# Optimization experiments

Measured on AMD Instinct MI355X. Metric: run time of the kernel, lower is better.

## Reference

```python
import jax, jax.numpy as jnp
import numpy as np

EMB_DIM = 512
R_DIM = 64
B, S = 8, 2048


def _lowrank_params(key):
    k1, k2, k3, k4 = jax.random.split(key, 4)
    s1 = 1.0 / np.sqrt(EMB_DIM)
    s2 = 1.0 / np.sqrt(R_DIM)
    w1 = jax.random.uniform(k1, (EMB_DIM, R_DIM), jnp.float32, -s1, s1)
    b1 = jax.random.uniform(k2, (R_DIM,), jnp.float32, -s1, s1)
    w2 = jax.random.uniform(k3, (R_DIM, EMB_DIM), jnp.float32, -s2, s2)
    b2 = jax.random.uniform(k4, (EMB_DIM,), jnp.float32, -s2, s2)
    return w1, b1, w2, b2


def setup_inputs() -> dict:
    key = jax.random.key(0)
    kx, km, kq, kk, kv = jax.random.split(key, 5)
    x = jax.random.normal(kx, (B, S, EMB_DIM), jnp.float32)
    attention_mask = jax.random.randint(km, (B, S), 0, 2, jnp.int32)
    q_w1, q_b1, q_w2, q_b2 = _lowrank_params(kq)
    k_w1, k_b1, k_w2, k_b2 = _lowrank_params(kk)
    v_w1, v_b1, v_w2, v_b2 = _lowrank_params(kv)
    return dict(x=x, attention_mask=attention_mask,
                q_w1=q_w1, q_b1=q_b1, q_w2=q_w2, q_b2=q_b2,
                k_w1=k_w1, k_b1=k_b1, k_w2=k_w2, k_b2=k_b2,
                v_w1=v_w1, v_b1=v_b1, v_w2=v_w2, v_b2=v_b2)


def _proj(x, w1, b1, w2, b2):
    # low-rank projection: emb -> r -> emb (two stacked Linears, no nonlinearity)
    return (x @ w1 + b1) @ w2 + b2


def reference(x, attention_mask,
              q_w1, q_b1, q_w2, q_b2,
              k_w1, k_b1, k_w2, k_b2,
              v_w1, v_b1, v_w2, v_b2):
    q = _proj(x, q_w1, q_b1, q_w2, q_b2)   # [B,S,E]
    k = _proj(x, k_w1, k_b1, k_w2, k_b2)   # [B,S,E]
    v = _proj(x, v_w1, v_b1, v_w2, v_b2)   # [B,S,E]
    scale = EMB_DIM ** (-0.5)
    scores = jnp.einsum('bse,bte->bst', q, k) * scale  # [B,S,S]
    m = attention_mask.astype(jnp.float32)
    scores = scores * m[:, :, None] * m[:, None, :]
    temp = jnp.einsum('bst,bte->bse', scores, v)       # [B,S,E]
    out = jax.nn.softmax(temp, axis=-1)                # softmax AFTER second bmm (non-standard)
    return out, q
```

## Files before the change

kernel.cpp:

```cpp
#include <hip/hip_runtime.h>
#include <hip/hip_bf16.h>

#define SCALE 0.044194173824159216f

typedef float f32x4 __attribute__((ext_vector_type(4)));
typedef __bf16 bf16x8 __attribute__((ext_vector_type(8)));

static __device__ __forceinline__ unsigned short f2bf(float f){
  unsigned u = __builtin_bit_cast(unsigned, f);
  u += 0x7fffu + ((u >> 16) & 1u);
  return (unsigned short)(u >> 16);
}

__global__ __launch_bounds__(256) void kA(const float* __restrict__ w1q, const float* __restrict__ w1k,
    const float* __restrict__ w1v, const float* __restrict__ w2q, const float* __restrict__ b2q,
    const float* __restrict__ w2k, const float* __restrict__ b2k,
    const float* __restrict__ w2v, const float* __restrict__ b2v,
    unsigned short* __restrict__ W1T, unsigned short* __restrict__ W2qT, float* __restrict__ Pm,
    unsigned short* __restrict__ Wvb){
  const int bid = blockIdx.x, t = threadIdx.x;
  if (bid < 64){
    #pragma unroll
    for (int s = 0; s < 8; s++){
      int id = s*16384 + bid*256 + t;
      if (id < 192*512){
        int n = id >> 9, k = id & 511;
        int p = n >> 6, c = n & 63;
        const float* w1 = (p==0)? w1q : ((p==1)? w1k : w1v);
        W1T[id] = f2bf(w1[k*64 + c]);
      } else {
        int j = id - 192*512;
        int e = j >> 6, r = j & 63;
        W2qT[j] = f2bf(w2q[r*512 + e]);
      }
    }
  } else if (bid < 81){
    int id = (bid - 64)*256 + t;
    if (id < 65*65){
      int i = id / 65, j = id - i*65;
      const float* qi = (i < 64)? (w2q + i*512) : b2q;
      const float* kj = (j < 64)? (w2k + j*512) : b2k;
      float s = 0.f;
      for (int e = 0; e < 512; e += 4){
        float4 a = *(const float4*)(qi + e);
        float4 b = *(const float4*)(kj + e);
        s += a.x*b.x + a.y*b.y + a.z*b.z + a.w*b.w;
      }
      Pm[id] = s * SCALE;
    }
  } else {
    int e = (bid - 81)*256 + t;
    unsigned short* wp = Wvb + e*96;
    for (int k = 0; k < 64; k++) wp[k] = f2bf(w2v[k*512 + e]);
    wp[64] = f2bf(b2v[e]);
    #pragma unroll
    for (int k = 65; k < 96; k++) wp[k] = 0;
  }
}

__global__ __launch_bounds__(256) void kB(const float* __restrict__ x, const unsigned short* __restrict__ W1T,
    const float* __restrict__ b1q, const float* __restrict__ b1k, const float* __restrict__ b1v,
    const int* __restrict__ mask,
    unsigned short* __restrict__ Hq, float* __restrict__ part){
  __shared__ __attribute__((aligned(16))) char smem[33792];
  unsigned short (*Ax)[40] = (unsigned short(*)[40])smem;
  unsigned short (*Bt)[40] = (unsigned short(*)[40])(smem + 5120);
  float (*ak)[66] = (float(*)[66])smem;
  float (*av)[66] = (float(*)[66])(smem + 16896);
  const int t = threadIdx.x;
  const int lane = t & 63, wave = t >> 6;
  const int l15 = lane & 15, lg = lane >> 4, ks = lg * 8;
  const int r0 = blockIdx.x * 64;
  f32x4 acc[12];
  #pragma unroll
  for (int j = 0; j < 12; j++) acc[j] = (f32x4){0.f,0.f,0.f,0.f};
  for (int k0 = 0; k0 < 512; k0 += 32){
    #pragma unroll
    for (int s = 0; s < 2; s++){
      int i = t + 256*s;
      int r = i >> 3, kq = (i & 7) * 4;
      float4 v = *(const float4*)(x + (size_t)(r0 + r)*512 + k0 + kq);
      ushort4 pk; pk.x = f2bf(v.x); pk.y = f2bf(v.y); pk.z = f2bf(v.z); pk.w = f2bf(v.w);
      *(ushort4*)&Ax[r][kq] = pk;
    }
    #pragma unroll
    for (int s = 0; s < 3; s++){
      int i = t + 256*s;
      int n = i >> 2, kq = (i & 3) * 8;
      *(uint4*)&Bt[n][kq] = *(const uint4*)(W1T + n*512 + k0 + kq);
    }
    __syncthreads();
    const int arow = (wave << 4) | l15;
    bf16x8 af = *(const bf16x8*)&Ax[arow][ks];
    #pragma unroll
    for (int j = 0; j < 12; j++){
      bf16x8 bf = *(const bf16x8*)&Bt[j*16 + l15][ks];
      acc[j] = __builtin_amdgcn_mfma_f32_16x16x32_bf16(af, bf, acc[j], 0, 0, 0);
    }
    __syncthreads();
  }
  int rowl[4]; float mrow[4];
  #pragma unroll
  for (int rg = 0; rg < 4; rg++){
    rowl[rg] = (wave << 4) + (lg << 2) + rg;
    mrow[rg] = (float)mask[r0 + rowl[rg]];
  }
  #pragma unroll
  for (int j = 0; j < 4; j++){
    int c = (j << 4) | l15;
    float bias = b1q[c];
    #pragma unroll
    for (int rg = 0; rg < 4; rg++)
      Hq[(size_t)(r0 + rowl[rg])*64 + c] = f2bf(acc[j][rg] + bias);
  }
  #pragma unroll
  for (int j = 0; j < 4; j++){
    int c = (j << 4) | l15;
    float bias = b1k[c];
    #pragma unroll
    for (int rg = 0; rg < 4; rg++)
      ak[rowl[rg]][c] = (acc[4 + j][rg] + bias) * mrow[rg];
  }
  #pragma unroll
  for (int j = 0; j < 4; j++){
    int c = (j << 4) | l15;
    float bias = b1v[c];
    #pragma unroll
    for (int rg = 0; rg < 4; rg++)
      av[rowl[rg]][c] = acc[8 + j][rg] + bias;
  }
  if (t < 64){ ak[t][64] = (float)mask[r0 + t]; av[t][64] = 1.f; }
  __syncthreads();
  if (t < 169){
    int tj = t / 13, ti = t - tj*13;
    int i0 = ti * 5, j0 = tj * 5;
    float pacc[5][5];
    #pragma unroll
    for (int a = 0; a < 5; a++)
      #pragma unroll
      for (int v = 0; v < 5; v++) pacc[a][v] = 0.f;
    for (int r = 0; r < 64; r++){
      float a[5], v[5];
      #pragma unroll
      for (int ii = 0; ii < 5; ii++) a[ii] = ak[r][i0 + ii];
      #pragma unroll
      for (int jj = 0; jj < 5; jj++) v[jj] = av[r][j0 + jj];
      #pragma unroll
      for (int ii = 0; ii < 5; ii++)
        #pragma unroll
        for (int jj = 0; jj < 5; jj++) pacc[ii][jj] += a[ii] * v[jj];
    }
    float* pout = part + (size_t)blockIdx.x * 4228;
    #pragma unroll
    for (int ii = 0; ii < 5; ii++)
      #pragma unroll
      for (int jj = 0; jj < 5; jj++)
        pout[(i0 + ii)*65 + (j0 + jj)] = pacc[ii][jj];
  }
}

__global__ __launch_bounds__(256) void kR2(const float* __restrict__ part, const float* __restrict__ Pm,
    unsigned short* __restrict__ T1bt, float* __restrict__ T1r64){
  __shared__ float Pl[65*66];
  __shared__ float Atl[4228];
  const int t = threadIdx.x, b = blockIdx.x;
  for (int id = t; id < 4225; id += 256){
    int i = id / 65, j = id - i*65;
    Pl[i*66 + j] = Pm[id];
  }
  const float* pb = part + (size_t)b*32*4228;
  for (int q = t; q < 1056; q += 256){
    f32x4 s0 = (f32x4){0.f,0.f,0.f,0.f}, s1 = s0, s2 = s0, s3 = s0;
    #pragma unroll
    for (int ch = 0; ch < 32; ch += 4){
      s0 += *(const f32x4*)(pb + (size_t)ch*4228     + q*4);
      s1 += *(const f32x4*)(pb + (size_t)(ch+1)*4228 + q*4);
      s2 += *(const f32x4*)(pb + (size_t)(ch+2)*4228 + q*4);
      s3 += *(const f32x4*)(pb + (size_t)(ch+3)*4228 + q*4);
    }
    *(f32x4*)&Atl[q*4] = (s0 + s1) + (s2 + s3);
  }
  if (t == 0){
    float s = 0.f;
    #pragma unroll
    for (int ch = 0; ch < 32; ch++) s += pb[(size_t)ch*4228 + 4224];
    Atl[4224] = s;
  }
  __syncthreads();
  unsigned short* Tb = T1bt + b*5120;
  float* Tr = T1r64 + b*80;
  if (t < 169){
    int tj = t / 13, ti = t - tj*13;
    int i0 = ti * 5, j0 = tj * 5;
    float acc[5][5];
    #pragma unroll
    for (int a = 0; a < 5; a++)
      #pragma unroll
      for (int v = 0; v < 5; v++) acc[a][v] = 0.f;
    for (int k = 0; k < 65; k++){
      float a[5], vv[5];
      #pragma unroll
      for (int ii = 0; ii < 5; ii++) a[ii] = Pl[(i0 + ii)*66 + k];
      #pragma unroll
      for (int jj = 0; jj < 5; jj++) vv[jj] = Atl[k*65 + j0 + jj];
      #pragma unroll
      for (int ii = 0; ii < 5; ii++)
        #pragma unroll
        for (int jj = 0; jj < 5; jj++) acc[ii][jj] += a[ii] * vv[jj];
    }
    #pragma unroll
    for (int ii = 0; ii < 5; ii++){
      int i = i0 + ii;
      #pragma unroll
      for (int jj = 0; jj < 5; jj++){
        int j = j0 + jj;
        if (i < 64) Tb[j*64 + i] = f2bf(acc[ii][jj]);
        else        Tr[j] = acc[ii][jj];
      }
    }
  }
  if (t < 240){
    int j = 65 + t/16, i4 = (t & 15) << 2;
    *(ushort4*)&Tb[j*64 + i4] = (ushort4){0,0,0,0};
  } else if (t < 255){
    Tr[65 + (t - 240)] = 0.f;
  }
}

__global__ __launch_bounds__(256) void kD2(const unsigned short* __restrict__ Hq,
    const unsigned short* __restrict__ W2qT, const unsigned short* __restrict__ T1bt,
    const float* __restrict__ T1r64, const unsigned short* __restrict__ Wvb,
    const float* __restrict__ b2q, const int* __restrict__ mask,
    float* __restrict__ out, float* __restrict__ qout){
  __shared__ __attribute__((aligned(16))) unsigned short t1l[64][104];
  const int t = threadIdx.x, lane = t & 63, wave = t >> 6;
  const int b = blockIdx.x >> 5, rc = (blockIdx.x & 31) << 6;
  const int l15 = lane & 15, lg = lane >> 4, ks = lg * 8;
  const size_t gr0 = (size_t)b*2048 + rc;
  const int arow = (wave << 4) | l15;
  const unsigned short* arp = Hq + (gr0 + arow)*64 + ks;
  bf16x8 a0 = *(const bf16x8*)arp;
  bf16x8 a1 = *(const bf16x8*)(arp + 32);
  const unsigned short* Tb = T1bt + b*5120;
  const float* Tr = T1r64 + b*80;
  f32x4 acc1[5];
  #pragma unroll
  for (int jf = 0; jf < 5; jf++) acc1[jf] = (f32x4){0.f,0.f,0.f,0.f};
  #pragma unroll
  for (int jf = 0; jf < 5; jf++){
    int col = (jf << 4) | l15;
    bf16x8 b0 = *(const bf16x8*)(Tb + col*64 + ks);
    bf16x8 b1 = *(const bf16x8*)(Tb + col*64 + 32 + ks);
    acc1[jf] = __builtin_amdgcn_mfma_f32_16x16x32_bf16(a0, b0, acc1[jf], 0, 0, 0);
    acc1[jf] = __builtin_amdgcn_mfma_f32_16x16x32_bf16(a1, b1, acc1[jf], 0, 0, 0);
  }
  *(ushort4*)&t1l[t >> 2][80 + ((t & 3) << 2)] = (ushort4){0,0,0,0};
  #pragma unroll
  for (int jf = 0; jf < 5; jf++){
    int col = (jf << 4) | l15;
    float tr = Tr[col];
    #pragma unroll
    for (int rg = 0; rg < 4; rg++)
      t1l[(wave << 4) + (lg << 2) + rg][col] = f2bf(acc1[jf][rg] + tr);
  }
  __syncthreads();
  bf16x8 c0 = *(const bf16x8*)&t1l[arow][ks];
  bf16x8 c1 = *(const bf16x8*)&t1l[arow][32 + ks];
  bf16x8 c2 = *(const bf16x8*)&t1l[arow][64 + ks];
  f32x4 acc[32];
  #pragma unroll
  for (int f = 0; f < 32; f++) acc[f] = (f32x4){0.f,0.f,0.f,0.f};
  #pragma unroll
  for (int f = 0; f < 32; f++){
    int col = (f << 4) | l15;
    const unsigned short* wp = Wvb + col*96;
    bf16x8 b0 = *(const bf16x8*)(wp + ks);
    bf16x8 b1 = *(const bf16x8*)(wp + 32 + ks);
    bf16x8 b2 = *(const bf16x8*)(wp + 64 + ks);
    acc[f] = __builtin_amdgcn_mfma_f32_16x16x32_bf16(c0, b0, acc[f], 0, 0, 0);
    acc[f] = __builtin_amdgcn_mfma_f32_16x16x32_bf16(c1, b1, acc[f], 0, 0, 0);
    acc[f] = __builtin_amdgcn_mfma_f32_16x16x32_bf16(c2, b2, acc[f], 0, 0, 0);
  }
  #pragma unroll
  for (int rg = 0; rg < 4; rg++){
    int row = rc + (wave << 4) + (lg << 2) + rg;
    float m = (float)mask[b*2048 + row];
    float mx = -3.4e38f;
    #pragma unroll
    for (int f = 0; f < 32; f++){
      float v = acc[f][rg] * m;
      acc[f][rg] = v;
      mx = fmaxf(mx, v);
    }
    #pragma unroll
    for (int d = 1; d < 16; d <<= 1) mx = fmaxf(mx, __shfl_xor(mx, d, 64));
    float sum = 0.f;
    #pragma unroll
    for (int f = 0; f < 32; f++){
      float ev = __expf(acc[f][rg] - mx);
      acc[f][rg] = ev;
      sum += ev;
    }
    #pragma unroll
    for (int d = 1; d < 16; d <<= 1) sum += __shfl_xor(sum, d, 64);
    float inv = 1.f / sum;
    float* orow = out + ((size_t)b*2048 + row) * 512;
    #pragma unroll
    for (int f = 0; f < 32; f++) orow[(f << 4) | l15] = acc[f][rg] * inv;
  }
  #pragma unroll
  for (int f = 0; f < 32; f++) acc[f] = (f32x4){0.f,0.f,0.f,0.f};
  #pragma unroll
  for (int f = 0; f < 32; f++){
    int col = (f << 4) | l15;
    bf16x8 b0 = *(const bf16x8*)(W2qT + col*64 + ks);
    bf16x8 b1 = *(const bf16x8*)(W2qT + col*64 + 32 + ks);
    acc[f] = __builtin_amdgcn_mfma_f32_16x16x32_bf16(a0, b0, acc[f], 0, 0, 0);
    acc[f] = __builtin_amdgcn_mfma_f32_16x16x32_bf16(a1, b1, acc[f], 0, 0, 0);
  }
  #pragma unroll
  for (int f = 0; f < 32; f++){
    int col = (f << 4) | l15;
    float bias = b2q[col];
    #pragma unroll
    for (int rg = 0; rg < 4; rg++){
      int row = rc + (wave << 4) + (lg << 2) + rg;
      qout[((size_t)b*2048 + row) * 512 + col] = acc[f][rg] + bias;
    }
  }
}

extern "C" void kernel_launch(void* const* d_in, const int* in_sizes, int n_in,
                              void* d_out, int out_size, void* d_ws, size_t ws_size,
                              hipStream_t stream){
  const float* x    = (const float*)d_in[0];
  const int*   mask = (const int*)d_in[1];
  const float* q_w1 = (const float*)d_in[2];
  const float* q_b1 = (const float*)d_in[3];
  const float* q_w2 = (const float*)d_in[4];
  const float* q_b2 = (const float*)d_in[5];
  const float* k_w1 = (const float*)d_in[6];
  const float* k_b1 = (const float*)d_in[7];
  const float* k_w2 = (const float*)d_in[8];
  const float* k_b2 = (const float*)d_in[9];
  const float* v_w1 = (const float*)d_in[10];
  const float* v_b1 = (const float*)d_in[11];
  const float* v_w2 = (const float*)d_in[12];
  const float* v_b2 = (const float*)d_in[13];

  char* ws = (char*)d_ws;
  unsigned short* W1T  = (unsigned short*)(ws + 0);
  unsigned short* W2qT = (unsigned short*)(ws + 196608);
  float*          Pm   = (float*)(ws + 262144);
  unsigned short* Hq   = (unsigned short*)(ws + 279296);
  float*          part = (float*)(ws + 2376448);
  unsigned short* Wvb  = (unsigned short*)(ws + 6705920);
  unsigned short* T1bt = (unsigned short*)(ws + 6804224);
  float*          T1r64= (float*)(ws + 6886144);

  float* out  = (float*)d_out;
  float* qout = out + (size_t)8*2048*512;

  kA <<<83,  256, 0, stream>>>(q_w1, k_w1, v_w1, q_w2, q_b2, k_w2, k_b2, v_w2, v_b2,
                               W1T, W2qT, Pm, Wvb);
  kB <<<256, 256, 0, stream>>>(x, W1T, q_b1, k_b1, v_b1, mask, Hq, part);
  kR2<<<8,   256, 0, stream>>>(part, Pm, T1bt, T1r64);
  kD2<<<256, 256, 0, stream>>>(Hq, W2qT, T1bt, T1r64, Wvb, q_b2, mask, out, qout);
}
```

Before: 93.65 us.

## Split reduction across many blocks and recompute small 65x65 product per block

```diff
diff --git a/kernel.cpp b/kernel.cpp
--- a/kernel.cpp
+++ b/kernel.cpp
@@ -10,6 +10,10 @@
   unsigned u = __builtin_bit_cast(unsigned, f);
   u += 0x7fffu + ((u >> 16) & 1u);
   return (unsigned short)(u >> 16);
+}
+static __device__ __forceinline__ __bf16 f2bfv(float f){
+  unsigned short s = f2bf(f);
+  return __builtin_bit_cast(__bf16, s);
 }
 
 __global__ __launch_bounds__(256) void kA(const float* __restrict__ w1q, const float* __restrict__ w1k,
@@ -159,80 +163,28 @@
   }
 }
 
-__global__ __launch_bounds__(256) void kR2(const float* __restrict__ part, const float* __restrict__ Pm,
-    unsigned short* __restrict__ T1bt, float* __restrict__ T1r64){
-  __shared__ float Pl[65*66];
-  __shared__ float Atl[4228];
-  const int t = threadIdx.x, b = blockIdx.x;
-  for (int id = t; id < 4225; id += 256){
-    int i = id / 65, j = id - i*65;
-    Pl[i*66 + j] = Pm[id];
-  }
-  const float* pb = part + (size_t)b*32*4228;
-  for (int q = t; q < 1056; q += 256){
-    f32x4 s0 = (f32x4){0.f,0.f,0.f,0.f}, s1 = s0, s2 = s0, s3 = s0;
-    #pragma unroll
-    for (int ch = 0; ch < 32; ch += 4){
-      s0 += *(const f32x4*)(pb + (size_t)ch*4228     + q*4);
-      s1 += *(const f32x4*)(pb + (size_t)(ch+1)*4228 + q*4);
-      s2 += *(const f32x4*)(pb + (size_t)(ch+2)*4228 + q*4);
-      s3 += *(const f32x4*)(pb + (size_t)(ch+3)*4228 + q*4);
-    }
-    *(f32x4*)&Atl[q*4] = (s0 + s1) + (s2 + s3);
-  }
-  if (t == 0){
+__global__ __launch_bounds__(256) void kR(const float* __restrict__ part, float* __restrict__ At){
+  int g = blockIdx.x*256 + threadIdx.x;
+  if (g < 33800){
+    int b = g / 4225, e = g - b*4225;
+    const float* p = part + (size_t)b*32*4228 + e;
     float s = 0.f;
     #pragma unroll
-    for (int ch = 0; ch < 32; ch++) s += pb[(size_t)ch*4228 + 4224];
-    Atl[4224] = s;
-  }
-  __syncthreads();
-  unsigned short* Tb = T1bt + b*5120;
-  float* Tr = T1r64 + b*80;
-  if (t < 169){
-    int tj = t / 13, ti = t - tj*13;
-    int i0 = ti * 5, j0 = tj * 5;
-    float acc[5][5];
-    #pragma unroll
-    for (int a = 0; a < 5; a++)
-      #pragma unroll
-      for (int v = 0; v < 5; v++) acc[a][v] = 0.f;
-    for (int k = 0; k < 65; k++){
-      float a[5], vv[5];
-      #pragma unroll
-      for (int ii = 0; ii < 5; ii++) a[ii] = Pl[(i0 + ii)*66 + k];
-      #pragma unroll
-      for (int jj = 0; jj < 5; jj++) vv[jj] = Atl[k*65 + j0 + jj];
-      #pragma unroll
-      for (int ii = 0; ii < 5; ii++)
-        #pragma unroll
-        for (int jj = 0; jj < 5; jj++) acc[ii][jj] += a[ii] * vv[jj];
-    }
-    #pragma unroll
-    for (int ii = 0; ii < 5; ii++){
-      int i = i0 + ii;
-      #pragma unroll
-      for (int jj = 0; jj < 5; jj++){
-        int j = j0 + jj;
-        if (i < 64) Tb[j*64 + i] = f2bf(acc[ii][jj]);
-        else        Tr[j] = acc[ii][jj];
-      }
-    }
-  }
-  if (t < 240){
-    int j = 65 + t/16, i4 = (t & 15) << 2;
-    *(ushort4*)&Tb[j*64 + i4] = (ushort4){0,0,0,0};
-  } else if (t < 255){
-    Tr[65 + (t - 240)] = 0.f;
-  }
-}
-
-__global__ __launch_bounds__(256) void kD2(const unsigned short* __restrict__ Hq,
-    const unsigned short* __restrict__ W2qT, const unsigned short* __restrict__ T1bt,
-    const float* __restrict__ T1r64, const unsigned short* __restrict__ Wvb,
+    for (int ch = 0; ch < 32; ch++) s += p[(size_t)ch*4228];
+    At[g] = s;
+  }
+}
+
+__global__ __launch_bounds__(256) void kDT(const unsigned short* __restrict__ Hq,
+    const unsigned short* __restrict__ W2qT, const float* __restrict__ At,
+    const float* __restrict__ Pm, const unsigned short* __restrict__ Wvb,
     const float* __restrict__ b2q, const int* __restrict__ mask,
     float* __restrict__ out, float* __restrict__ qout){
-  __shared__ __attribute__((aligned(16))) unsigned short t1l[64][104];
+  __shared__ __attribute__((aligned(16))) char smem[51712];
+  float* Pl  = (float*)smem;
+  float* Atl = (float*)(smem + 17160);
+  float* T1l = (float*)(smem + 34320);
+  unsigned short (*t1l)[104] = (unsigned short(*)[104])smem;
   const int t = threadIdx.x, lane = t & 63, wave = t >> 6;
   const int b = blockIdx.x >> 5, rc = (blockIdx.x & 31) << 6;
   const int l15 = lane & 15, lg = lane >> 4, ks = lg * 8;
@@ -241,27 +193,68 @@
   const unsigned short* arp = Hq + (gr0 + arow)*64 + ks;
   bf16x8 a0 = *(const bf16x8*)arp;
   bf16x8 a1 = *(const bf16x8*)(arp + 32);
-  const unsigned short* Tb = T1bt + b*5120;
-  const float* Tr = T1r64 + b*80;
+  for (int id = t; id < 4225; id += 256){
+    int i = id / 65, j = id - i*65;
+    Pl[i*66 + j]  = Pm[id];
+    Atl[i*66 + j] = At[(size_t)b*4225 + id];
+  }
+  __syncthreads();
+  if (t < 169){
+    int tj = t / 13, ti = t - tj*13;
+    int i0 = ti * 5, j0 = tj * 5;
+    float acc[5][5];
+    #pragma unroll
+    for (int a = 0; a < 5; a++)
+      #pragma unroll
+      for (int v = 0; v < 5; v++) acc[a][v] = 0.f;
+    for (int k = 0; k < 65; k++){
+      float a[5], vv[5];
+      #pragma unroll
+      for (int ii = 0; ii < 5; ii++) a[ii] = Pl[(i0 + ii)*66 + k];
+      #pragma unroll
+      for (int jj = 0; jj < 5; jj++) vv[jj] = Atl[k*66 + j0 + jj];
+      #pragma unroll
+      for (int ii = 0; ii < 5; ii++)
+        #pragma unroll
+        for (int jj = 0; jj < 5; jj++) acc[ii][jj] += a[ii] * vv[jj];
+    }
+    #pragma unroll
+    for (int ii = 0; ii < 5; ii++)
+      #pragma unroll
+      for (int jj = 0; jj < 5; jj++) T1l[(i0 + ii)*66 + (j0 + jj)] = acc[ii][jj];
+  }
+  __syncthreads();
   f32x4 acc1[5];
   #pragma unroll
-  for (int jf = 0; jf < 5; jf++) acc1[jf] = (f32x4){0.f,0.f,0.f,0.f};
-  #pragma unroll
-  for (int jf = 0; jf < 5; jf++){
-    int col = (jf << 4) | l15;
-    bf16x8 b0 = *(const bf16x8*)(Tb + col*64 + ks);
-    bf16x8 b1 = *(const bf16x8*)(Tb + col*64 + 32 + ks);
-    acc1[jf] = __builtin_amdgcn_mfma_f32_16x16x32_bf16(a0, b0, acc1[jf], 0, 0, 0);
-    acc1[jf] = __builtin_amdgcn_mfma_f32_16x16x32_bf16(a1, b1, acc1[jf], 0, 0, 0);
-  }
+  for (int f = 0; f < 5; f++) acc1[f] = (f32x4){0.f,0.f,0.f,0.f};
+  float trow[5];
+  #pragma unroll
+  for (int f = 0; f < 5; f++){
+    int j = (f << 4) | l15;
+    bf16x8 b0, b1;
+    if (j < 65){
+      #pragma unroll
+      for (int idx = 0; idx < 8; idx++){
+        b0[idx] = f2bfv(T1l[(ks + idx)*66 + j]);
+        b1[idx] = f2bfv(T1l[(32 + ks + idx)*66 + j]);
+      }
+      trow[f] = T1l[64*66 + j];
+    } else {
+      #pragma unroll
+      for (int idx = 0; idx < 8; idx++){ b0[idx] = f2bfv(0.f); b1[idx] = f2bfv(0.f); }
+      trow[f] = 0.f;
+    }
+    acc1[f] = __builtin_amdgcn_mfma_f32_16x16x32_bf16(a0, b0, acc1[f], 0, 0, 0);
+    acc1[f] = __builtin_amdgcn_mfma_f32_16x16x32_bf16(a1, b1, acc1[f], 0, 0, 0);
+  }
+  __syncthreads();
   *(ushort4*)&t1l[t >> 2][80 + ((t & 3) << 2)] = (ushort4){0,0,0,0};
   #pragma unroll
-  for (int jf = 0; jf < 5; jf++){
-    int col = (jf << 4) | l15;
-    float tr = Tr[col];
+  for (int f = 0; f < 5; f++){
+    int j = (f << 4) | l15;
     #pragma unroll
     for (int rg = 0; rg < 4; rg++)
-      t1l[(wave << 4) + (lg << 2) + rg][col] = f2bf(acc1[jf][rg] + tr);
+      t1l[(wave << 4) + (lg << 2) + rg][j] = f2bf(acc1[f][rg] + trow[f]);
   }
   __syncthreads();
   bf16x8 c0 = *(const bf16x8*)&t1l[arow][ks];
@@ -354,9 +347,8 @@
   float*          Pm   = (float*)(ws + 262144);
   unsigned short* Hq   = (unsigned short*)(ws + 279296);
   float*          part = (float*)(ws + 2376448);
-  unsigned short* Wvb  = (unsigned short*)(ws + 6705920);
-  unsigned short* T1bt = (unsigned short*)(ws + 6804224);
-  float*          T1r64= (float*)(ws + 6886144);
+  float*          At   = (float*)(ws + 6705920);
+  unsigned short* Wvb  = (unsigned short*)(ws + 6841344);
 
   float* out  = (float*)d_out;
   float* qout = out + (size_t)8*2048*512;
@@ -364,6 +356,6 @@
   kA <<<83,  256, 0, stream>>>(q_w1, k_w1, v_w1, q_w2, q_b2, k_w2, k_b2, v_w2, v_b2,
                                W1T, W2qT, Pm, Wvb);
   kB <<<256, 256, 0, stream>>>(x, W1T, q_b1, k_b1, v_b1, mask, Hq, part);
-  kR2<<<8,   256, 0, stream>>>(part, Pm, T1bt, T1r64);
-  kD2<<<256, 256, 0, stream>>>(Hq, W2qT, T1bt, T1r64, Wvb, q_b2, mask, out, qout);
-}
+  kR <<<133, 256, 0, stream>>>(part, At);
+  kDT<<<256, 256, 0, stream>>>(Hq, W2qT, At, Pm, Wvb, q_b2, mask, out, qout);
+}
```

Measured after the change: 92.30 us. About the same (-1.4%).

## Split partial reduction and T1 product across 136 blocks with chunk-major layout

Applied to the files above, without the earlier changes.

```diff
diff --git a/kernel.cpp b/kernel.cpp
--- a/kernel.cpp
+++ b/kernel.cpp
@@ -150,80 +150,59 @@
         #pragma unroll
         for (int jj = 0; jj < 5; jj++) pacc[ii][jj] += a[ii] * v[jj];
     }
-    float* pout = part + (size_t)blockIdx.x * 4228;
+    float* pout = part + ((size_t)(blockIdx.x >> 5) * 4225) * 32 + (blockIdx.x & 31);
     #pragma unroll
     for (int ii = 0; ii < 5; ii++)
       #pragma unroll
       for (int jj = 0; jj < 5; jj++)
-        pout[(i0 + ii)*65 + (j0 + jj)] = pacc[ii][jj];
-  }
-}
-
-__global__ __launch_bounds__(256) void kR2(const float* __restrict__ part, const float* __restrict__ Pm,
+        pout[(size_t)((i0 + ii)*65 + (j0 + jj)) * 32] = pacc[ii][jj];
+  }
+}
+
+__global__ __launch_bounds__(256) void kRT1(const float* __restrict__ part, const float* __restrict__ Pm,
     unsigned short* __restrict__ T1bt, float* __restrict__ T1r64){
   __shared__ float Pl[65*66];
-  __shared__ float Atl[4228];
-  const int t = threadIdx.x, b = blockIdx.x;
+  __shared__ float Avl[65*4];
+  const int t = threadIdx.x;
+  const int b = blockIdx.x / 17, jc = blockIdx.x - b*17;
   for (int id = t; id < 4225; id += 256){
     int i = id / 65, j = id - i*65;
     Pl[i*66 + j] = Pm[id];
   }
-  const float* pb = part + (size_t)b*32*4228;
-  for (int q = t; q < 1056; q += 256){
-    f32x4 s0 = (f32x4){0.f,0.f,0.f,0.f}, s1 = s0, s2 = s0, s3 = s0;
-    #pragma unroll
-    for (int ch = 0; ch < 32; ch += 4){
-      s0 += *(const f32x4*)(pb + (size_t)ch*4228     + q*4);
-      s1 += *(const f32x4*)(pb + (size_t)(ch+1)*4228 + q*4);
-      s2 += *(const f32x4*)(pb + (size_t)(ch+2)*4228 + q*4);
-      s3 += *(const f32x4*)(pb + (size_t)(ch+3)*4228 + q*4);
-    }
-    *(f32x4*)&Atl[q*4] = (s0 + s1) + (s2 + s3);
-  }
-  if (t == 0){
-    float s = 0.f;
-    #pragma unroll
-    for (int ch = 0; ch < 32; ch++) s += pb[(size_t)ch*4228 + 4224];
-    Atl[4224] = s;
+  const int ncol = (jc < 16) ? 4 : 1;
+  const int j0 = jc * 4;
+  const int nel = 65 * ncol;
+  for (int z = t; z < nel; z += 256){
+    int k = z / ncol, jj = z - k*ncol;
+    const float* p = part + ((size_t)b*4225 + k*65 + (j0 + jj)) * 32;
+    f32x4 s0 = *(const f32x4*)(p);       f32x4 s1 = *(const f32x4*)(p + 4);
+    f32x4 s2 = *(const f32x4*)(p + 8);   f32x4 s3 = *(const f32x4*)(p + 12);
+    s0 += *(const f32x4*)(p + 16); s1 += *(const f32x4*)(p + 20);
+    s2 += *(const f32x4*)(p + 24); s3 += *(const f32x4*)(p + 28);
+    f32x4 s = (s0 + s1) + (s2 + s3);
+    Avl[k*4 + jj] = s[0] + s[1] + s[2] + s[3];
   }
   __syncthreads();
   unsigned short* Tb = T1bt + b*5120;
   float* Tr = T1r64 + b*80;
-  if (t < 169){
-    int tj = t / 13, ti = t - tj*13;
-    int i0 = ti * 5, j0 = tj * 5;
-    float acc[5][5];
-    #pragma unroll
-    for (int a = 0; a < 5; a++)
-      #pragma unroll
-      for (int v = 0; v < 5; v++) acc[a][v] = 0.f;
-    for (int k = 0; k < 65; k++){
-      float a[5], vv[5];
-      #pragma unroll
-      for (int ii = 0; ii < 5; ii++) a[ii] = Pl[(i0 + ii)*66 + k];
-      #pragma unroll
-      for (int jj = 0; jj < 5; jj++) vv[jj] = Atl[k*65 + j0 + jj];
-      #pragma unroll
-      for (int ii = 0; ii < 5; ii++)
-        #pragma unroll
-        for (int jj = 0; jj < 5; jj++) acc[ii][jj] += a[ii] * vv[jj];
-    }
-    #pragma unroll
-    for (int ii = 0; ii < 5; ii++){
-      int i = i0 + ii;
-      #pragma unroll
-      for (int jj = 0; jj < 5; jj++){
-        int j = j0 + jj;
-        if (i < 64) Tb[j*64 + i] = f2bf(acc[ii][jj]);
-        else        Tr[j] = acc[ii][jj];
+  for (int z = t; z < nel; z += 256){
+    int i = z / ncol, jj = z - i*ncol;
+    int j = j0 + jj;
+    float s = 0.f;
+    #pragma unroll 13
+    for (int k = 0; k < 65; k++) s += Pl[i*66 + k] * Avl[k*4 + jj];
+    if (i < 64) Tb[j*64 + i] = f2bf(s);
+    else        Tr[j] = s;
+  }
+  if (jc == 16){
+    for (int z = t; z < 255; z += 256){
+      if (z < 240){
+        int j = 65 + z/16, i4 = (z & 15) << 2;
+        *(ushort4*)&Tb[j*64 + i4] = (ushort4){0,0,0,0};
+      } else {
+        Tr[65 + (z - 240)] = 0.f;
       }
     }
-  }
-  if (t < 240){
-    int j = 65 + t/16, i4 = (t & 15) << 2;
-    *(ushort4*)&Tb[j*64 + i4] = (ushort4){0,0,0,0};
-  } else if (t < 255){
-    Tr[65 + (t - 240)] = 0.f;
   }
 }
 
@@ -354,16 +333,16 @@
   float*          Pm   = (float*)(ws + 262144);
   unsigned short* Hq   = (unsigned short*)(ws + 279296);
   float*          part = (float*)(ws + 2376448);
-  unsigned short* Wvb  = (unsigned short*)(ws + 6705920);
-  unsigned short* T1bt = (unsigned short*)(ws + 6804224);
-  float*          T1r64= (float*)(ws + 6886144);
+  unsigned short* Wvb  = (unsigned short*)(ws + 6702848);
+  unsigned short* T1bt = (unsigned short*)(ws + 6801152);
+  float*          T1r64= (float*)(ws + 6883072);
 
   float* out  = (float*)d_out;
   float* qout = out + (size_t)8*2048*512;
 
-  kA <<<83,  256, 0, stream>>>(q_w1, k_w1, v_w1, q_w2, q_b2, k_w2, k_b2, v_w2, v_b2,
-                               W1T, W2qT, Pm, Wvb);
-  kB <<<256, 256, 0, stream>>>(x, W1T, q_b1, k_b1, v_b1, mask, Hq, part);
-  kR2<<<8,   256, 0, stream>>>(part, Pm, T1bt, T1r64);
-  kD2<<<256, 256, 0, stream>>>(Hq, W2qT, T1bt, T1r64, Wvb, q_b2, mask, out, qout);
-}
+  kA  <<<83,  256, 0, stream>>>(q_w1, k_w1, v_w1, q_w2, q_b2, k_w2, k_b2, v_w2, v_b2,
+                                W1T, W2qT, Pm, Wvb);
+  kB  <<<256, 256, 0, stream>>>(x, W1T, q_b1, k_b1, v_b1, mask, Hq, part);
+  kRT1<<<136, 256, 0, stream>>>(part, Pm, T1bt, T1r64);
+  kD2 <<<256, 256, 0, stream>>>(Hq, W2qT, T1bt, T1r64, Wvb, q_b2, mask, out, qout);
+}
```

After: 90.14 us. 1.04x faster.
